# Kernel tuning notes

Measured on AMD Instinct MI355X. Metric: run time of the kernel, lower is better.

The kernel has to match this reference:

```python
import jax, jax.numpy as jnp
import numpy as np

B, S, E, H = 2, 2048, 1024, 16
D = E // H  # head_dim = 64


def setup_inputs() -> dict:
    key = jax.random.key(0)
    ks = jax.random.split(key, 9)
    s = 1.0 / np.sqrt(E)
    return {
        "x": jax.random.normal(ks[0], (B, S, E), dtype=jnp.float32),
        "Wq": jax.random.uniform(ks[1], (E, E), jnp.float32, -s, s),
        "bq": jax.random.uniform(ks[2], (E,), jnp.float32, -s, s),
        "Wk": jax.random.uniform(ks[3], (E, E), jnp.float32, -s, s),
        "bk": jax.random.uniform(ks[4], (E,), jnp.float32, -s, s),
        "Wv": jax.random.uniform(ks[5], (E, E), jnp.float32, -s, s),
        "bv": jax.random.uniform(ks[6], (E,), jnp.float32, -s, s),
        "Wo": jax.random.uniform(ks[7], (E, E), jnp.float32, -s, s),
        "bo": jax.random.uniform(ks[8], (E,), jnp.float32, -s, s),
    }


def reference(x, Wq, bq, Wk, bk, Wv, bv, Wo, bo):
    # QKV projections (torch Linear: x @ W.T + b), split into heads: [B,H,S,D]
    def proj(t, W, b):
        return (t @ W.T + b).reshape(B, S, H, D).transpose(0, 2, 1, 3)

    Q = proj(x, Wq, bq)
    K = proj(x, Wk, bk)
    V = proj(x, Wv, bv)
    # scores [B,H,S,S], scaled by sqrt(head_dim)
    score = jnp.einsum('bnqd,bnkd->bnqk', Q, K) / jnp.sqrt(jnp.float32(D))
    weights = jax.nn.softmax(score, axis=-1)
    out = jnp.einsum('bnql,bnld->bnqd', weights, V)  # [B,H,S,D]
    out = out.transpose(0, 2, 1, 3).reshape(B, S, E)
    return out @ Wo.T + bo
```

## Files before the change

kernel.cpp:

```cpp
#include <hip/hip_runtime.h>


#define B_ 2
#define S_ 2048
#define E_ 1024
#define H_ 16
#define D_ 64
#define M_ (B_ * S_)

typedef __attribute__((ext_vector_type(8))) _Float16 f16x8;
typedef __attribute__((ext_vector_type(4))) _Float16 f16x4;
typedef __attribute__((ext_vector_type(4))) float f32x4;
typedef __attribute__((ext_vector_type(8))) unsigned short u16x8;

#define LOG2E  1.44269504f
#define CLOG2  4.32808512f

static __device__ __forceinline__ float bf16_to_f32(unsigned short u) {
    return __uint_as_float(((unsigned)u) << 16);
}
static __device__ __forceinline__ unsigned short f32_to_bf16(float f) {
    unsigned u = __float_as_uint(f);
    u += 0x7FFFu + ((u >> 16) & 1u);
    return (unsigned short)(u >> 16);
}
static __device__ __forceinline__ float load1_f32(const void* p, int i, bool isbf) {
    return isbf ? bf16_to_f32(((const unsigned short*)p)[i]) : ((const float*)p)[i];
}
static __device__ __forceinline__ void store1(void* p, size_t i, float v, bool isbf) {
    if (isbf) ((unsigned short*)p)[i] = f32_to_bf16(v);
    else      ((float*)p)[i] = v;
}
static __device__ __forceinline__ void gl2lds16(const void* g, void* l) {
    __builtin_amdgcn_global_load_lds((const __attribute__((address_space(1))) unsigned int*)g,
                                     (__attribute__((address_space(3))) unsigned int*)l, 16, 0, 0);
}

__global__ void detect_dtype(const unsigned short* __restrict__ x, int* __restrict__ flag) {
    const int lane = threadIdx.x;
    const unsigned short h = x[2 * lane];
    const int e = (h >> 7) & 0xFF;
    const bool sane = (e >= 0x60 && e <= 0x9F);
    const unsigned long long m = __ballot(sane);
    if (lane == 0) *flag = (__popcll(m) >= 48) ? 1 : 0;
}

__global__ __launch_bounds__(256) void convert_inputs(
    const void* __restrict__ x,  const void* __restrict__ wq,
    const void* __restrict__ wk, const void* __restrict__ wv,
    const void* __restrict__ wo, const int* __restrict__ flag,
    _Float16* __restrict__ x16, _Float16* __restrict__ w16)
{
    const bool isbf = (*flag != 0);
    const size_t t = ((size_t)blockIdx.x * 256 + threadIdx.x) * 8;
    const void* src; size_t off; _Float16* dst; float scale = 1.0f;
    if (t < (size_t)M_ * E_) { src = x; off = t; dst = x16 + t; }
    else {
        const size_t u = t - (size_t)M_ * E_;
        const int wsel = (int)(u >> 20);
        off = u & ((1u << 20) - 1);
        src = wsel == 0 ? wq : wsel == 1 ? wk : wsel == 2 ? wv : wo;
        dst = w16 + u;
        if (wsel == 0) scale = 0.125f * LOG2E;
    }
    f16x8 v;
    if (isbf) {
        u16x8 s = *(const u16x8*)((const unsigned short*)src + off);
        #pragma unroll
        for (int j = 0; j < 8; ++j) v[j] = (_Float16)(bf16_to_f32(s[j]) * scale);
    } else {
        const float* f = (const float*)src + off;
        f32x4 lo = *(const f32x4*)f;
        f32x4 hi = *(const f32x4*)(f + 4);
        #pragma unroll
        for (int j = 0; j < 4; ++j) {
            v[j]     = (_Float16)(lo[j] * scale);
            v[4 + j] = (_Float16)(hi[j] * scale);
        }
    }
    *(f16x8*)dst = v;
}

__global__ __launch_bounds__(256) void gemm_qkv(
    const _Float16* __restrict__ x16, const _Float16* __restrict__ w16,
    const void* __restrict__ bq, const void* __restrict__ bk, const void* __restrict__ bv,
    const int* __restrict__ flag,
    _Float16* __restrict__ Qb, _Float16* __restrict__ Kb, _Float16* __restrict__ VTb)
{
    __shared__ __align__(16) _Float16 As[128 * 32];
    __shared__ __align__(16) _Float16 Bs[128 * 32];
    const bool isbf = (*flag != 0);
    const int tid = threadIdx.x, wave = tid >> 6, lane = tid & 63;
    const int wm = wave >> 1, wn = wave & 1;
    const int qd = lane >> 4, ln = lane & 15;
    const int m0 = blockIdx.x * 128;
    const int by = blockIdx.y;
    const int wsel = by >> 3;
    const int n0 = (by & 7) * 128;
    const _Float16* W = w16 + ((size_t)wsel << 20);

    const int i0 = wave * 64 + lane;
    const int i1 = i0 + 256;
    const _Float16* ga0 = x16 + (size_t)(m0 + (i0 >> 2)) * E_ + (i0 & 3) * 8;
    const _Float16* ga1 = x16 + (size_t)(m0 + (i1 >> 2)) * E_ + (i1 & 3) * 8;
    const _Float16* gb0 = W + (size_t)(n0 + (i0 >> 2)) * E_ + (i0 & 3) * 8;
    const _Float16* gb1 = W + (size_t)(n0 + (i1 >> 2)) * E_ + (i1 & 3) * 8;
    char* lA0 = (char*)As + (size_t)(wave * 64) * 16;
    char* lA1 = (char*)As + (size_t)(wave * 64 + 256) * 16;
    char* lB0 = (char*)Bs + (size_t)(wave * 64) * 16;
    char* lB1 = (char*)Bs + (size_t)(wave * 64 + 256) * 16;

    const _Float16* aS = (wsel == 2) ? Bs : As;
    const _Float16* bS = (wsel == 2) ? As : Bs;

    f32x4 acc[16] = {};

    for (int kt = 0; kt < E_; kt += 32) {
        __syncthreads();
        gl2lds16(ga0 + kt, lA0);
        gl2lds16(ga1 + kt, lA1);
        gl2lds16(gb0 + kt, lB0);
        gl2lds16(gb1 + kt, lB1);
        __syncthreads();
        f16x8 a[4], b[4];
        #pragma unroll
        for (int mt = 0; mt < 4; ++mt)
            a[mt] = *(const f16x8*)&aS[(wm * 64 + mt * 16 + ln) * 32 + qd * 8];
        #pragma unroll
        for (int nt = 0; nt < 4; ++nt)
            b[nt] = *(const f16x8*)&bS[(wn * 64 + nt * 16 + ln) * 32 + qd * 8];
        #pragma unroll
        for (int mt = 0; mt < 4; ++mt)
            #pragma unroll
            for (int nt = 0; nt < 4; ++nt)
                acc[mt * 4 + nt] = __builtin_amdgcn_mfma_f32_16x16x32_f16(a[mt], b[nt], acc[mt * 4 + nt], 0, 0, 0);
    }

    if (wsel != 2) {
        const void* bias = wsel == 0 ? bq : bk;
        const float bscale = (wsel == 0) ? 0.125f * LOG2E : 1.0f;
        _Float16* dst = wsel == 0 ? Qb : Kb;
        #pragma unroll
        for (int nt = 0; nt < 4; ++nt) {
            const int n = n0 + wn * 64 + nt * 16 + ln;
            const float bvv = load1_f32(bias, n, isbf) * bscale;
            const int h = n >> 6, d = n & 63;
            #pragma unroll
            for (int mt = 0; mt < 4; ++mt)
                #pragma unroll
                for (int r = 0; r < 4; ++r) {
                    const int m = m0 + wm * 64 + mt * 16 + qd * 4 + r;
                    const int b = m >> 11, s = m & (S_ - 1);
                    dst[((size_t)(b * H_ + h) * S_ + s) * D_ + d] =
                        (_Float16)(acc[mt * 4 + nt][r] + bvv);
                }
        }
    } else {
        #pragma unroll
        for (int mt = 0; mt < 4; ++mt)
            #pragma unroll
            for (int r = 0; r < 4; ++r) {
                const int e = n0 + wm * 64 + mt * 16 + qd * 4 + r;
                const float bvv = load1_f32(bv, e, isbf);
                const int h = e >> 6, d = e & 63;
                #pragma unroll
                for (int nt = 0; nt < 4; ++nt) {
                    const int sg = m0 + wn * 64 + nt * 16 + ln;
                    const int b = sg >> 11, s = sg & (S_ - 1);
                    VTb[((size_t)(b * H_ + h) * D_ + d) * S_ + s] =
                        (_Float16)(acc[mt * 4 + nt][r] + bvv);
                }
            }
    }
}

__global__ __launch_bounds__(256) void attn(
    const _Float16* __restrict__ Q, const _Float16* __restrict__ K,
    const _Float16* __restrict__ VT, _Float16* __restrict__ AO)
{
    __shared__ __align__(16) _Float16 Ks[2][64][72];
    __shared__ __align__(16) _Float16 Ps[128][72];

    const int tid = threadIdx.x, wave = tid >> 6, lane = tid & 63;
    const int qd = lane >> 4, ln = lane & 15;
    const int L = blockIdx.x;
    const int bh = ((L & 7) << 2) | ((L >> 3) & 3);
    const int qt = L >> 5;
    const int b = bh >> 4, h = bh & (H_ - 1);

    const _Float16* Kbase = K + (size_t)bh * S_ * D_;
    const _Float16* Vbase = VT + (size_t)bh * D_ * S_;

    f16x8 qf[2][2];
    #pragma unroll
    for (int g = 0; g < 2; ++g) {
        const _Float16* qrow = Q + ((size_t)bh * S_ + qt * 128 + wave * 32 + g * 16 + ln) * D_;
        qf[g][0] = *(const f16x8*)(qrow + qd * 8);
        qf[g][1] = *(const f16x8*)(qrow + 32 + qd * 8);
    }

    f16x8 ones;
    #pragma unroll
    for (int j = 0; j < 8; ++j) ones[j] = (_Float16)1.0f;

    f32x4 o[2][4] = {};
    f32x4 li2[2] = {};

    const int sr = tid >> 2, sc0 = (tid & 3) * 16;
    const _Float16* kp = Kbase + (size_t)sr * D_ + sc0;
    const _Float16* vp[2][4];
    #pragma unroll
    for (int kk = 0; kk < 2; ++kk)
        #pragma unroll
        for (int dt = 0; dt < 4; ++dt)
            vp[kk][dt] = Vbase + (size_t)(dt * 16 + ln) * S_ + kk * 32 + qd * 8;

    *(f16x8*)&Ks[0][sr][sc0]     = *(const f16x8*)kp;
    *(f16x8*)&Ks[0][sr][sc0 + 8] = *(const f16x8*)(kp + 8);
    kp += 64 * D_;
    __syncthreads();

    for (int kt = 0; kt < S_; kt += 64) {
        const int p = (kt >> 6) & 1;

        f16x8 vf[2][4];
        #pragma unroll
        for (int kk = 0; kk < 2; ++kk)
            #pragma unroll
            for (int dt = 0; dt < 4; ++dt) {
                vf[kk][dt] = *(const f16x8*)vp[kk][dt];
                vp[kk][dt] += 64;
            }

        const bool more = (kt + 64) < S_;
        f16x8 kn0, kn1;
        if (more) {
            kn0 = *(const f16x8*)kp;
            kn1 = *(const f16x8*)(kp + 8);
            kp += 64 * D_;
        }

        f16x8 af[2][4];
        #pragma unroll
        for (int kk = 0; kk < 2; ++kk)
            #pragma unroll
            for (int t4 = 0; t4 < 4; ++t4)
                af[kk][t4] = *(const f16x8*)&Ks[p][t4 * 16 + ln][kk * 32 + qd * 8];

        #pragma unroll
        for (int g = 0; g < 2; ++g) {
            f32x4 sc[4] = {};
            #pragma unroll
            for (int kk = 0; kk < 2; ++kk)
                #pragma unroll
                for (int t4 = 0; t4 < 4; ++t4)
                    sc[t4] = __builtin_amdgcn_mfma_f32_16x16x32_f16(af[kk][t4], qf[g][kk], sc[t4], 0, 0, 0);

            #pragma unroll
            for (int t4 = 0; t4 < 4; ++t4) {
                f16x4 ph;
                #pragma unroll
                for (int r = 0; r < 4; ++r)
                    ph[r] = (_Float16)exp2f(sc[t4][r] - CLOG2);
                *(f16x4*)&Ps[wave * 32 + g * 16 + ln][t4 * 16 + qd * 4] = ph;
            }
        }

        #pragma unroll
        for (int g = 0; g < 2; ++g)
            #pragma unroll
            for (int kk = 0; kk < 2; ++kk) {
                f16x8 pf = *(const f16x8*)&Ps[wave * 32 + g * 16 + ln][kk * 32 + qd * 8];
                #pragma unroll
                for (int dt = 0; dt < 4; ++dt)
                    o[g][dt] = __builtin_amdgcn_mfma_f32_16x16x32_f16(pf, vf[kk][dt], o[g][dt], 0, 0, 0);
                li2[g] = __builtin_amdgcn_mfma_f32_16x16x32_f16(pf, ones, li2[g], 0, 0, 0);
            }

        if (more) {
            *(f16x8*)&Ks[p ^ 1][sr][sc0]     = kn0;
            *(f16x8*)&Ks[p ^ 1][sr][sc0 + 8] = kn1;
        }
        __syncthreads();
    }

    #pragma unroll
    for (int g = 0; g < 2; ++g)
        #pragma unroll
        for (int r = 0; r < 4; ++r) {
            const float inv = 1.0f / li2[g][r];
            const int s = qt * 128 + wave * 32 + g * 16 + qd * 4 + r;
            #pragma unroll
            for (int dt = 0; dt < 4; ++dt)
                AO[((size_t)b * S_ + s) * E_ + h * D_ + dt * 16 + ln] = (_Float16)(o[g][dt][r] * inv);
        }
}

__global__ __launch_bounds__(256) void gemm_out(
    const _Float16* __restrict__ A, const _Float16* __restrict__ W,
    const void* __restrict__ bias, const int* __restrict__ flag, void* __restrict__ out)
{
    __shared__ __align__(16) _Float16 As[128 * 32];
    __shared__ __align__(16) _Float16 Bs[128 * 32];
    const bool isbf = (*flag != 0);
    const int tid = threadIdx.x, wave = tid >> 6, lane = tid & 63;
    const int wm = wave >> 1, wn = wave & 1;
    const int qd = lane >> 4, ln = lane & 15;
    const int m0 = blockIdx.x * 128;
    const int n0 = blockIdx.y * 128;

    const int i0 = wave * 64 + lane;
    const int i1 = i0 + 256;
    const _Float16* ga0 = A + (size_t)(m0 + (i0 >> 2)) * E_ + (i0 & 3) * 8;
    const _Float16* ga1 = A + (size_t)(m0 + (i1 >> 2)) * E_ + (i1 & 3) * 8;
    const _Float16* gb0 = W + (size_t)(n0 + (i0 >> 2)) * E_ + (i0 & 3) * 8;
    const _Float16* gb1 = W + (size_t)(n0 + (i1 >> 2)) * E_ + (i1 & 3) * 8;
    char* lA0 = (char*)As + (size_t)(wave * 64) * 16;
    char* lA1 = (char*)As + (size_t)(wave * 64 + 256) * 16;
    char* lB0 = (char*)Bs + (size_t)(wave * 64) * 16;
    char* lB1 = (char*)Bs + (size_t)(wave * 64 + 256) * 16;

    f32x4 acc[16] = {};

    for (int kt = 0; kt < E_; kt += 32) {
        __syncthreads();
        gl2lds16(ga0 + kt, lA0);
        gl2lds16(ga1 + kt, lA1);
        gl2lds16(gb0 + kt, lB0);
        gl2lds16(gb1 + kt, lB1);
        __syncthreads();
        f16x8 a[4], b[4];
        #pragma unroll
        for (int mt = 0; mt < 4; ++mt)
            a[mt] = *(const f16x8*)&As[(wm * 64 + mt * 16 + ln) * 32 + qd * 8];
        #pragma unroll
        for (int nt = 0; nt < 4; ++nt)
            b[nt] = *(const f16x8*)&Bs[(wn * 64 + nt * 16 + ln) * 32 + qd * 8];
        #pragma unroll
        for (int mt = 0; mt < 4; ++mt)
            #pragma unroll
            for (int nt = 0; nt < 4; ++nt)
                acc[mt * 4 + nt] = __builtin_amdgcn_mfma_f32_16x16x32_f16(a[mt], b[nt], acc[mt * 4 + nt], 0, 0, 0);
    }

    #pragma unroll
    for (int nt = 0; nt < 4; ++nt) {
        const int n = n0 + wn * 64 + nt * 16 + ln;
        const float bvv = load1_f32(bias, n, isbf);
        #pragma unroll
        for (int mt = 0; mt < 4; ++mt)
            #pragma unroll
            for (int r = 0; r < 4; ++r) {
                const int m = m0 + wm * 64 + mt * 16 + qd * 4 + r;
                store1(out, (size_t)m * E_ + n, acc[mt * 4 + nt][r] + bvv, isbf);
            }
    }
}

extern "C" void kernel_launch(void* const* d_in, const int* in_sizes, int n_in,
                              void* d_out, int out_size, void* d_ws, size_t ws_size,
                              hipStream_t stream) {
    const void* x  = d_in[0];
    const void* Wq = d_in[1];
    const void* bq = d_in[2];
    const void* Wk = d_in[3];
    const void* bk = d_in[4];
    const void* Wv = d_in[5];
    const void* bv = d_in[6];
    const void* Wo = d_in[7];
    const void* bo = d_in[8];

    int* flag = (int*)d_ws;
    _Float16* x16 = (_Float16*)((char*)d_ws + 1024);
    _Float16* w16 = x16 + (size_t)M_ * E_;
    _Float16* Qb  = w16 + 4u * (size_t)E_ * E_;
    _Float16* Kb  = Qb + (size_t)M_ * E_;
    _Float16* VTb = Kb + (size_t)M_ * E_;
    _Float16* AO  = x16;

    detect_dtype<<<1, 64, 0, stream>>>((const unsigned short*)x, flag);
    convert_inputs<<<4096, 256, 0, stream>>>(x, Wq, Wk, Wv, Wo, flag, x16, w16);
    gemm_qkv<<<dim3(32, 24), 256, 0, stream>>>(x16, w16, bq, bk, bv, flag, Qb, Kb, VTb);
    attn<<<512, 256, 0, stream>>>(Qb, Kb, VTb, AO);
    gemm_out<<<dim3(32, 8), 256, 0, stream>>>(AO, w16 + 3u * (size_t)E_ * E_, bo, flag, d_out);
}
```

Before: 228.3 us.

## Widen GEMM K-tiles with swizzled LDS, enlarge attention K tiles, fuse dtype detection

Both GEMMs now stage 64-wide K slices per barrier pair instead of 32, using an XOR-style column swizzle in LDS to avoid bank conflicts, which halves the number of sync rounds. The attention kernel double-buffers 128-key K tiles and processes them in two 64-key halves, so it syncs half as often. Its exp2 is replaced by a raw v_exp_f32 with packed round-toward-zero fp16 conversion. The separate dtype-detection launch is folded into the convert kernel, at the cost of every block redundantly recomputing the flag and using more LDS per block.

```diff
diff --git a/kernel.cpp b/kernel.cpp
--- a/kernel.cpp
+++ b/kernel.cpp
@@ -10,6 +10,7 @@
 
 typedef __attribute__((ext_vector_type(8))) _Float16 f16x8;
 typedef __attribute__((ext_vector_type(4))) _Float16 f16x4;
+typedef __attribute__((ext_vector_type(2))) _Float16 f16x2;
 typedef __attribute__((ext_vector_type(4))) float f32x4;
 typedef __attribute__((ext_vector_type(8))) unsigned short u16x8;
 
@@ -35,24 +36,38 @@
     __builtin_amdgcn_global_load_lds((const __attribute__((address_space(1))) unsigned int*)g,
                                      (__attribute__((address_space(3))) unsigned int*)l, 16, 0, 0);
 }
-
-__global__ void detect_dtype(const unsigned short* __restrict__ x, int* __restrict__ flag) {
-    const int lane = threadIdx.x;
-    const unsigned short h = x[2 * lane];
-    const int e = (h >> 7) & 0xFF;
-    const bool sane = (e >= 0x60 && e <= 0x9F);
-    const unsigned long long m = __ballot(sane);
-    if (lane == 0) *flag = (__popcll(m) >= 48) ? 1 : 0;
+static __device__ __forceinline__ float rexp2(float x) {
+    float r;
+    asm("v_exp_f32 %0, %1" : "=v"(r) : "v"(x));
+    return r;
+}
+static __device__ __forceinline__ f16x4 pack4(float e0, float e1, float e2, float e3) {
+    f16x2 lo = __builtin_bit_cast(f16x2, __builtin_amdgcn_cvt_pkrtz(e0, e1));
+    f16x2 hi = __builtin_bit_cast(f16x2, __builtin_amdgcn_cvt_pkrtz(e2, e3));
+    return __builtin_shufflevector(lo, hi, 0, 1, 2, 3);
 }
 
 __global__ __launch_bounds__(256) void convert_inputs(
     const void* __restrict__ x,  const void* __restrict__ wq,
     const void* __restrict__ wk, const void* __restrict__ wv,
-    const void* __restrict__ wo, const int* __restrict__ flag,
-    _Float16* __restrict__ x16, _Float16* __restrict__ w16)
+    const void* __restrict__ wo,
+    _Float16* __restrict__ x16, _Float16* __restrict__ w16,
+    int* __restrict__ flag_out)
 {
-    const bool isbf = (*flag != 0);
-    const size_t t = ((size_t)blockIdx.x * 256 + threadIdx.x) * 8;
+    __shared__ int sflag;
+    const int tid = threadIdx.x;
+    if (tid < 64) {
+        const unsigned short hh = ((const unsigned short*)x)[2 * tid];
+        const int e = (hh >> 7) & 0xFF;
+        const bool sane = (e >= 0x60 && e <= 0x9F);
+        const unsigned long long m = __ballot(sane);
+        if (tid == 0) sflag = (__popcll(m) >= 48) ? 1 : 0;
+    }
+    __syncthreads();
+    const bool isbf = sflag != 0;
+    if (blockIdx.x == 0 && tid == 0) *flag_out = sflag;
+
+    const size_t t = ((size_t)blockIdx.x * 256 + tid) * 8;
     const void* src; size_t off; _Float16* dst; float scale = 1.0f;
     if (t < (size_t)M_ * E_) { src = x; off = t; dst = x16 + t; }
     else {
@@ -87,8 +102,8 @@
     const int* __restrict__ flag,
     _Float16* __restrict__ Qb, _Float16* __restrict__ Kb, _Float16* __restrict__ VTb)
 {
-    __shared__ __align__(16) _Float16 As[128 * 32];
-    __shared__ __align__(16) _Float16 Bs[128 * 32];
+    __shared__ __align__(16) _Float16 As[128 * 64];
+    __shared__ __align__(16) _Float16 Bs[128 * 64];
     const bool isbf = (*flag != 0);
     const int tid = threadIdx.x, wave = tid >> 6, lane = tid & 63;
     const int wm = wave >> 1, wn = wave & 1;
@@ -99,41 +114,51 @@
     const int n0 = (by & 7) * 128;
     const _Float16* W = w16 + ((size_t)wsel << 20);
 
-    const int i0 = wave * 64 + lane;
-    const int i1 = i0 + 256;
-    const _Float16* ga0 = x16 + (size_t)(m0 + (i0 >> 2)) * E_ + (i0 & 3) * 8;
-    const _Float16* ga1 = x16 + (size_t)(m0 + (i1 >> 2)) * E_ + (i1 & 3) * 8;
-    const _Float16* gb0 = W + (size_t)(n0 + (i0 >> 2)) * E_ + (i0 & 3) * 8;
-    const _Float16* gb1 = W + (size_t)(n0 + (i1 >> 2)) * E_ + (i1 & 3) * 8;
-    char* lA0 = (char*)As + (size_t)(wave * 64) * 16;
-    char* lA1 = (char*)As + (size_t)(wave * 64 + 256) * 16;
-    char* lB0 = (char*)Bs + (size_t)(wave * 64) * 16;
-    char* lB1 = (char*)Bs + (size_t)(wave * 64 + 256) * 16;
-
-    const _Float16* aS = (wsel == 2) ? Bs : As;
-    const _Float16* bS = (wsel == 2) ? As : Bs;
+    char* dX = (wsel == 2) ? (char*)Bs : (char*)As;
+    char* dW = (wsel == 2) ? (char*)As : (char*)Bs;
+
+    const _Float16* gx[4]; const _Float16* gw[4];
+    char* lx[4]; char* lw[4];
+    #pragma unroll
+    for (int it = 0; it < 4; ++it) {
+        const int seg = it * 256 + tid;
+        const int row = seg >> 3, cg = seg & 7;
+        const int scol = ((cg + row) & 7) * 8;
+        gx[it] = x16 + (size_t)(m0 + row) * E_ + scol;
+        gw[it] = W + (size_t)(n0 + row) * E_ + scol;
+        lx[it] = dX + (size_t)(it * 256 + wave * 64) * 16;
+        lw[it] = dW + (size_t)(it * 256 + wave * 64) * 16;
+    }
+
+    const int sw0 = ((qd - ln) & 7) * 8;
+    const int sw1 = ((qd + 4 - ln) & 7) * 8;
 
     f32x4 acc[16] = {};
 
-    for (int kt = 0; kt < E_; kt += 32) {
+    for (int kt = 0; kt < E_; kt += 64) {
         __syncthreads();
-        gl2lds16(ga0 + kt, lA0);
-        gl2lds16(ga1 + kt, lA1);
-        gl2lds16(gb0 + kt, lB0);
-        gl2lds16(gb1 + kt, lB1);
+        #pragma unroll
+        for (int it = 0; it < 4; ++it) {
+            gl2lds16(gx[it] + kt, lx[it]);
+            gl2lds16(gw[it] + kt, lw[it]);
+        }
         __syncthreads();
-        f16x8 a[4], b[4];
-        #pragma unroll
-        for (int mt = 0; mt < 4; ++mt)
-            a[mt] = *(const f16x8*)&aS[(wm * 64 + mt * 16 + ln) * 32 + qd * 8];
-        #pragma unroll
-        for (int nt = 0; nt < 4; ++nt)
-            b[nt] = *(const f16x8*)&bS[(wn * 64 + nt * 16 + ln) * 32 + qd * 8];
-        #pragma unroll
-        for (int mt = 0; mt < 4; ++mt)
+        #pragma unroll
+        for (int kk = 0; kk < 2; ++kk) {
+            const int sw = kk ? sw1 : sw0;
+            f16x8 a[4], bfr[4];
+            #pragma unroll
+            for (int mt = 0; mt < 4; ++mt)
+                a[mt] = *(const f16x8*)&As[((wm * 64 + mt * 16 + ln) << 6) + sw];
             #pragma unroll
             for (int nt = 0; nt < 4; ++nt)
-                acc[mt * 4 + nt] = __builtin_amdgcn_mfma_f32_16x16x32_f16(a[mt], b[nt], acc[mt * 4 + nt], 0, 0, 0);
+                bfr[nt] = *(const f16x8*)&Bs[((wn * 64 + nt * 16 + ln) << 6) + sw];
+            #pragma unroll
+            for (int mt = 0; mt < 4; ++mt)
+                #pragma unroll
+                for (int nt = 0; nt < 4; ++nt)
+                    acc[mt * 4 + nt] = __builtin_amdgcn_mfma_f32_16x16x32_f16(a[mt], bfr[nt], acc[mt * 4 + nt], 0, 0, 0);
+        }
     }
 
     if (wsel != 2) {
@@ -178,7 +203,7 @@
     const _Float16* __restrict__ Q, const _Float16* __restrict__ K,
     const _Float16* __restrict__ VT, _Float16* __restrict__ AO)
 {
-    __shared__ __align__(16) _Float16 Ks[2][64][72];
+    __shared__ __align__(16) _Float16 Ks[2][128][72];
     __shared__ __align__(16) _Float16 Ps[128][72];
 
     const int tid = threadIdx.x, wave = tid >> 6, lane = tid & 63;
@@ -206,80 +231,75 @@
     f32x4 o[2][4] = {};
     f32x4 li2[2] = {};
 
-    const int sr = tid >> 2, sc0 = (tid & 3) * 16;
+    const int sr = tid >> 1, sc0 = (tid & 1) * 32;
     const _Float16* kp = Kbase + (size_t)sr * D_ + sc0;
-    const _Float16* vp[2][4];
-    #pragma unroll
-    for (int kk = 0; kk < 2; ++kk)
-        #pragma unroll
-        for (int dt = 0; dt < 4; ++dt)
-            vp[kk][dt] = Vbase + (size_t)(dt * 16 + ln) * S_ + kk * 32 + qd * 8;
-
-    *(f16x8*)&Ks[0][sr][sc0]     = *(const f16x8*)kp;
-    *(f16x8*)&Ks[0][sr][sc0 + 8] = *(const f16x8*)(kp + 8);
-    kp += 64 * D_;
+    #pragma unroll
+    for (int j = 0; j < 4; ++j)
+        *(f16x8*)&Ks[0][sr][sc0 + j * 8] = *(const f16x8*)(kp + j * 8);
+    kp += 128 * D_;
     __syncthreads();
 
-    for (int kt = 0; kt < S_; kt += 64) {
-        const int p = (kt >> 6) & 1;
-
-        f16x8 vf[2][4];
-        #pragma unroll
-        for (int kk = 0; kk < 2; ++kk)
-            #pragma unroll
-            for (int dt = 0; dt < 4; ++dt) {
-                vf[kk][dt] = *(const f16x8*)vp[kk][dt];
-                vp[kk][dt] += 64;
+    for (int kt = 0; kt < S_; kt += 128) {
+        const int p = (kt >> 7) & 1;
+        const bool more = (kt + 128) < S_;
+        f16x8 kn[4];
+        if (more) {
+            #pragma unroll
+            for (int j = 0; j < 4; ++j) kn[j] = *(const f16x8*)(kp + j * 8);
+            kp += 128 * D_;
+        }
+
+        #pragma unroll
+        for (int hf = 0; hf < 2; ++hf) {
+            const int kb = kt + hf * 64;
+
+            f16x8 vf[2][4];
+            #pragma unroll
+            for (int kk = 0; kk < 2; ++kk)
+                #pragma unroll
+                for (int dt = 0; dt < 4; ++dt)
+                    vf[kk][dt] = *(const f16x8*)(Vbase + (size_t)(dt * 16 + ln) * S_ + kb + kk * 32 + qd * 8);
+
+            f16x8 af[2][4];
+            #pragma unroll
+            for (int kk = 0; kk < 2; ++kk)
+                #pragma unroll
+                for (int t4 = 0; t4 < 4; ++t4)
+                    af[kk][t4] = *(const f16x8*)&Ks[p][hf * 64 + t4 * 16 + ln][kk * 32 + qd * 8];
+
+            #pragma unroll
+            for (int g = 0; g < 2; ++g) {
+                f32x4 sc[4] = {};
+                #pragma unroll
+                for (int kk = 0; kk < 2; ++kk)
+                    #pragma unroll
+                    for (int t4 = 0; t4 < 4; ++t4)
+                        sc[t4] = __builtin_amdgcn_mfma_f32_16x16x32_f16(af[kk][t4], qf[g][kk], sc[t4], 0, 0, 0);
+
+                #pragma unroll
+                for (int t4 = 0; t4 < 4; ++t4) {
+                    f16x4 ph = pack4(rexp2(sc[t4][0] - CLOG2), rexp2(sc[t4][1] - CLOG2),
+                                     rexp2(sc[t4][2] - CLOG2), rexp2(sc[t4][3] - CLOG2));
+                    *(f16x4*)&Ps[wave * 32 + g * 16 + ln][t4 * 16 + qd * 4] = ph;
+                }
             }
 
-        const bool more = (kt + 64) < S_;
-        f16x8 kn0, kn1;
+            #pragma unroll
+            for (int g = 0; g < 2; ++g)
+                #pragma unroll
+                for (int kk = 0; kk < 2; ++kk) {
+                    f16x8 pf = *(const f16x8*)&Ps[wave * 32 + g * 16 + ln][kk * 32 + qd * 8];
+                    #pragma unroll
+                    for (int dt = 0; dt < 4; ++dt)
+                        o[g][dt] = __builtin_amdgcn_mfma_f32_16x16x32_f16(pf, vf[kk][dt], o[g][dt], 0, 0, 0);
+                    li2[g] = __builtin_amdgcn_mfma_f32_16x16x32_f16(pf, ones, li2[g], 0, 0, 0);
+                }
+        }
+
         if (more) {
-            kn0 = *(const f16x8*)kp;
-            kn1 = *(const f16x8*)(kp + 8);
-            kp += 64 * D_;
-        }
-
-        f16x8 af[2][4];
-        #pragma unroll
-        for (int kk = 0; kk < 2; ++kk)
-            #pragma unroll
-            for (int t4 = 0; t4 < 4; ++t4)
-                af[kk][t4] = *(const f16x8*)&Ks[p][t4 * 16 + ln][kk * 32 + qd * 8];
-
-        #pragma unroll
-        for (int g = 0; g < 2; ++g) {
-            f32x4 sc[4] = {};
-            #pragma unroll
-            for (int kk = 0; kk < 2; ++kk)
-                #pragma unroll
-                for (int t4 = 0; t4 < 4; ++t4)
-                    sc[t4] = __builtin_amdgcn_mfma_f32_16x16x32_f16(af[kk][t4], qf[g][kk], sc[t4], 0, 0, 0);
-
-            #pragma unroll
-            for (int t4 = 0; t4 < 4; ++t4) {
-                f16x4 ph;
-                #pragma unroll
-                for (int r = 0; r < 4; ++r)
-                    ph[r] = (_Float16)exp2f(sc[t4][r] - CLOG2);
-                *(f16x4*)&Ps[wave * 32 + g * 16 + ln][t4 * 16 + qd * 4] = ph;
-            }
-        }
-
-        #pragma unroll
-        for (int g = 0; g < 2; ++g)
-            #pragma unroll
-            for (int kk = 0; kk < 2; ++kk) {
-                f16x8 pf = *(const f16x8*)&Ps[wave * 32 + g * 16 + ln][kk * 32 + qd * 8];
-                #pragma unroll
-                for (int dt = 0; dt < 4; ++dt)
-                    o[g][dt] = __builtin_amdgcn_mfma_f32_16x16x32_f16(pf, vf[kk][dt], o[g][dt], 0, 0, 0);
-                li2[g] = __builtin_amdgcn_mfma_f32_16x16x32_f16(pf, ones, li2[g], 0, 0, 0);
-            }
-
-        if (more) {
-            *(f16x8*)&Ks[p ^ 1][sr][sc0]     = kn0;
-            *(f16x8*)&Ks[p ^ 1][sr][sc0 + 8] = kn1;
+            #pragma unroll
+            for (int j = 0; j < 4; ++j)
+                *(f16x8*)&Ks[p ^ 1][sr][sc0 + j * 8] = kn[j];
         }
         __syncthreads();
     }
@@ -300,8 +320,8 @@
     const _Float16* __restrict__ A, const _Float16* __restrict__ W,
     const void* __restrict__ bias, const int* __restrict__ flag, void* __restrict__ out)
 {
-    __shared__ __align__(16) _Float16 As[128 * 32];
-    __shared__ __align__(16) _Float16 Bs[128 * 32];
+    __shared__ __align__(16) _Float16 As[128 * 64];
+    __shared__ __align__(16) _Float16 Bs[128 * 64];
     const bool isbf = (*flag != 0);
     const int tid = threadIdx.x, wave = tid >> 6, lane = tid & 63;
     const int wm = wave >> 1, wn = wave & 1;
@@ -309,38 +329,47 @@
     const int m0 = blockIdx.x * 128;
     const int n0 = blockIdx.y * 128;
 
-    const int i0 = wave * 64 + lane;
-    const int i1 = i0 + 256;
-    const _Float16* ga0 = A + (size_t)(m0 + (i0 >> 2)) * E_ + (i0 & 3) * 8;
-    const _Float16* ga1 = A + (size_t)(m0 + (i1 >> 2)) * E_ + (i1 & 3) * 8;
-    const _Float16* gb0 = W + (size_t)(n0 + (i0 >> 2)) * E_ + (i0 & 3) * 8;
-    const _Float16* gb1 = W + (size_t)(n0 + (i1 >> 2)) * E_ + (i1 & 3) * 8;
-    char* lA0 = (char*)As + (size_t)(wave * 64) * 16;
-    char* lA1 = (char*)As + (size_t)(wave * 64 + 256) * 16;
-    char* lB0 = (char*)Bs + (size_t)(wave * 64) * 16;
-    char* lB1 = (char*)Bs + (size_t)(wave * 64 + 256) * 16;
+    const _Float16* ga[4]; const _Float16* gb[4];
+    char* la[4]; char* lb[4];
+    #pragma unroll
+    for (int it = 0; it < 4; ++it) {
+        const int seg = it * 256 + tid;
+        const int row = seg >> 3, cg = seg & 7;
+        const int scol = ((cg + row) & 7) * 8;
+        ga[it] = A + (size_t)(m0 + row) * E_ + scol;
+        gb[it] = W + (size_t)(n0 + row) * E_ + scol;
+        la[it] = (char*)As + (size_t)(it * 256 + wave * 64) * 16;
+        lb[it] = (char*)Bs + (size_t)(it * 256 + wave * 64) * 16;
+    }
+    const int sw0 = ((qd - ln) & 7) * 8;
+    const int sw1 = ((qd + 4 - ln) & 7) * 8;
 
     f32x4 acc[16] = {};
 
-    for (int kt = 0; kt < E_; kt += 32) {
+    for (int kt = 0; kt < E_; kt += 64) {
         __syncthreads();
-        gl2lds16(ga0 + kt, lA0);
-        gl2lds16(ga1 + kt, lA1);
-        gl2lds16(gb0 + kt, lB0);
-        gl2lds16(gb1 + kt, lB1);
+        #pragma unroll
+        for (int it = 0; it < 4; ++it) {
+            gl2lds16(ga[it] + kt, la[it]);
+            gl2lds16(gb[it] + kt, lb[it]);
+        }
         __syncthreads();
-        f16x8 a[4], b[4];
-        #pragma unroll
-        for (int mt = 0; mt < 4; ++mt)
-            a[mt] = *(const f16x8*)&As[(wm * 64 + mt * 16 + ln) * 32 + qd * 8];
-        #pragma unroll
-        for (int nt = 0; nt < 4; ++nt)
-            b[nt] = *(const f16x8*)&Bs[(wn * 64 + nt * 16 + ln) * 32 + qd * 8];
-        #pragma unroll
-        for (int mt = 0; mt < 4; ++mt)
+        #pragma unroll
+        for (int kk = 0; kk < 2; ++kk) {
+            const int sw = kk ? sw1 : sw0;
+            f16x8 a[4], bfr[4];
+            #pragma unroll
+            for (int mt = 0; mt < 4; ++mt)
+                a[mt] = *(const f16x8*)&As[((wm * 64 + mt * 16 + ln) << 6) + sw];
             #pragma unroll
             for (int nt = 0; nt < 4; ++nt)
-                acc[mt * 4 + nt] = __builtin_amdgcn_mfma_f32_16x16x32_f16(a[mt], b[nt], acc[mt * 4 + nt], 0, 0, 0);
+                bfr[nt] = *(const f16x8*)&Bs[((wn * 64 + nt * 16 + ln) << 6) + sw];
+            #pragma unroll
+            for (int mt = 0; mt < 4; ++mt)
+                #pragma unroll
+                for (int nt = 0; nt < 4; ++nt)
+                    acc[mt * 4 + nt] = __builtin_amdgcn_mfma_f32_16x16x32_f16(a[mt], bfr[nt], acc[mt * 4 + nt], 0, 0, 0);
+        }
     }
 
     #pragma unroll
@@ -378,8 +407,7 @@
     _Float16* VTb = Kb + (size_t)M_ * E_;
     _Float16* AO  = x16;
 
-    detect_dtype<<<1, 64, 0, stream>>>((const unsigned short*)x, flag);
-    convert_inputs<<<4096, 256, 0, stream>>>(x, Wq, Wk, Wv, Wo, flag, x16, w16);
+    convert_inputs<<<4096, 256, 0, stream>>>(x, Wq, Wk, Wv, Wo, x16, w16, flag);
     gemm_qkv<<<dim3(32, 24), 256, 0, stream>>>(x16, w16, bq, bk, bv, flag, Qb, Kb, VTb);
     attn<<<512, 256, 0, stream>>>(Qb, Kb, VTb, AO);
     gemm_out<<<dim3(32, 8), 256, 0, stream>>>(AO, w16 + 3u * (size_t)E_ * E_, bo, flag, d_out);
```

Result: faster. 217.6 us (-4.7%).
